# Performance work log

Measured on AMD Instinct MI355X. Metric: run time of the kernel, lower is better.

Reference implementation:

```python
import jax, jax.numpy as jnp
import numpy as np


def _gather_neighbours(h, idx):
    # h: (B, N, H); idx: (B, N, K) int -> (B, N, K, H)
    B, N, H = h.shape
    K = idx.shape[-1]
    flat = idx.reshape(B, N * K)  # (B, N*K)
    rep = jnp.take_along_axis(h, flat[..., None], axis=1)  # (B, N*K, H)
    return rep.reshape(B, N, K, H)


def _masked_agg(h, idx, mask):
    # gather neighbor hidden states then masked sum over neighbors -> (B, N, H)
    rep = _gather_neighbours(h, idx)
    return jnp.einsum('bnkh,bnk->bnh', rep, mask)


def setup_inputs() -> dict:
    key = jax.random.key(0)
    ks = jax.random.split(key, 12)
    B, N, H, K = 8, 2000, 128, 32
    s = 1.0 / np.sqrt(H)
    return {
        'node_hidden': jax.random.normal(ks[0], (B, N, H), jnp.float32),
        'cell': jax.random.normal(ks[1], (B, N, H), jnp.float32),
        'w_in': jax.random.normal(ks[2], (4, H, H), jnp.float32) * s,
        'w_out': jax.random.normal(ks[3], (4, H, H), jnp.float32) * s,
        'u_in': jax.random.normal(ks[4], (4, H, H), jnp.float32) * s,
        'u_out': jax.random.normal(ks[5], (4, H, H), jnp.float32) * s,
        'b': jax.random.normal(ks[6], (4, H), jnp.float32) * 0.1,
        'in_node_mask': jax.random.uniform(ks[7], (B, N, K), jnp.float32),
        'out_node_mask': jax.random.uniform(ks[8], (B, N, K), jnp.float32),
        'in_node_index': jax.random.randint(ks[9], (B, N, K), 0, N, jnp.int32),
        'out_node_index': jax.random.randint(ks[10], (B, N, K), 0, N, jnp.int32),
        'layer_num': 2,
    }


def reference(node_hidden, cell, w_in, w_out, u_in, u_out, b,
              in_node_mask, out_node_mask, in_node_index, out_node_index,
              layer_num):
    h, c = node_hidden, cell
    for _ in range(layer_num):
        in_agg = _masked_agg(h, in_node_index, in_node_mask)    # (B,N,H)
        out_agg = _masked_agg(h, out_node_index, out_node_mask)  # (B,N,H)
        # gate pre-activations, gate order: i, o, f, cell
        pre = (jnp.einsum('bnh,ghd->gbnd', in_agg, w_in)
               + jnp.einsum('bnh,ghd->gbnd', out_agg, w_out)
               + jnp.einsum('bnh,ghd->gbnd', h, u_in)
               + jnp.einsum('bnh,ghd->gbnd', h, u_out)
               + b[:, None, None, :])
        i_g = jax.nn.sigmoid(pre[0])
        o_g = jax.nn.sigmoid(pre[1])
        f_g = jax.nn.sigmoid(pre[2])
        g = jnp.tanh(pre[3])
        c = f_g * c + i_g * g
        h = o_g * jnp.tanh(c)
    return h
```

## Files before the change

kernel.cpp:

```cpp
#include <hip/hip_runtime.h>
#include <math.h>

#define B_ 8
#define N_ 2000
#define H_ 128
#define K_ 32
#define M_ (B_*N_)
#define KTOT 384
#define NC 512
#define NTILES 32
#define NCHUNK 12
#define AGG_BLOCKS (M_ / 8)
#define PREP_BLOCKS (NTILES * NCHUNK)

typedef __attribute__((ext_vector_type(8))) short s8_t;
typedef __attribute__((ext_vector_type(4))) float f4_t;

__device__ __forceinline__ unsigned short f2bf(float x) {
    union { float f; unsigned u; } v; v.f = x;
    unsigned r = v.u + 0x7fff + ((v.u >> 16) & 1);
    return (unsigned short)(r >> 16);
}
__device__ __forceinline__ float bf2f(unsigned short b) {
    union { unsigned u; float f; } v; v.u = (unsigned)b << 16; return v.f;
}
__device__ __forceinline__ float sigm_(float x) { return 1.f / (1.f + __expf(-x)); }
__device__ __forceinline__ float tanh_(float x) { return 2.f / (1.f + __expf(-2.f * x)) - 1.f; }

__device__ __forceinline__ float pickv(f4_t A, int m) {
    float ab = (m & 1) ? A.y : A.x;
    float cd = (m & 1) ? A.w : A.z;
    return (m & 2) ? cd : ab;
}
__device__ __forceinline__ float pick4(float u0, float u1, float u2, float u3, int m) {
    float ab = (m & 1) ? u1 : u0;
    float cd = (m & 1) ? u3 : u2;
    return (m & 2) ? cd : ab;
}

__device__ __forceinline__ void split4(const float* f, ushort4& hi, ushort4& lo) {
    unsigned short h0 = f2bf(f[0]), h1 = f2bf(f[1]), h2 = f2bf(f[2]), h3 = f2bf(f[3]);
    hi = make_ushort4(h0, h1, h2, h3);
    lo = make_ushort4(f2bf(f[0] - bf2f(h0)), f2bf(f[1] - bf2f(h1)),
                      f2bf(f[2] - bf2f(h2)), f2bf(f[3] - bf2f(h3)));
}

__device__ __forceinline__ void gload_lds(const unsigned short* g, short* l) {
    __builtin_amdgcn_global_load_lds(
        (const __attribute__((address_space(1))) unsigned*)g,
        (__attribute__((address_space(3))) unsigned*)l, 16, 0, 0);
}


__device__ __forceinline__ void prep_elem(int pb, int t,
                                          const float* __restrict__ w_in,
                                          const float* __restrict__ w_out,
                                          const float* __restrict__ u_in,
                                          const float* __restrict__ u_out,
                                          unsigned short* __restrict__ wp_hi,
                                          unsigned short* __restrict__ wp_lo) {
    int ntile = pb / NCHUNK, chunk = pb % NCHUNK;
    int lane = t >> 3, e = t & 7;
    int col = ntile * 16 + (lane & 15);
    int k = chunk * 32 + (lane >> 4) * 8 + e;
    int d = col >> 2, g = col & 3;
    float v;
    if (k < 128) {
        v = w_in[(g * 128 + k) * 128 + d];
    } else if (k < 256) {
        v = w_out[(g * 128 + (k - 128)) * 128 + d];
    } else {
        int kk = k - 256;
        v = u_in[(g * 128 + kk) * 128 + d] + u_out[(g * 128 + kk) * 128 + d];
    }
    unsigned short hs = f2bf(v);
    wp_hi[(size_t)pb * 512 + t] = hs;
    wp_lo[(size_t)pb * 512 + t] = f2bf(v - bf2f(hs));
}

__device__ __forceinline__ void agg_body(int bid, int tid,
                                         const float* __restrict__ h,
                                         const int* __restrict__ in_idx,
                                         const float* __restrict__ in_mask,
                                         const int* __restrict__ out_idx,
                                         const float* __restrict__ out_mask,
                                         unsigned short* __restrict__ A_hi,
                                         unsigned short* __restrict__ A_lo,
                                         int (*s_idx)[64], float (*s_msk)[64]) {
    int r = tid >> 5;
    int p = tid & 31;
    int row = bid * 8 + r;
    int b = row / N_;
    const float* hb = h + (size_t)b * N_ * H_;

    for (int e = tid; e < 512; e += 256) {
        int r2 = e >> 6, q = e & 63;
        int ridx = bid * 8 + r2;
        if (q < 32) {
            s_idx[r2][q] = in_idx[ridx * K_ + q];
            s_msk[r2][q] = in_mask[ridx * K_ + q];
        } else {
            s_idx[r2][q] = out_idx[ridx * K_ + (q - 32)];
            s_msk[r2][q] = out_mask[ridx * K_ + (q - 32)];
        }
    }
    __syncthreads();

    int d0 = p * 4;
    float ai[4] = {0.f, 0.f, 0.f, 0.f};
    float ao[4] = {0.f, 0.f, 0.f, 0.f};
    #pragma unroll 16
    for (int k = 0; k < K_; ++k) {
        int   i1 = s_idx[r][k];
        float m1 = s_msk[r][k];
        int   i2 = s_idx[r][32 + k];
        float m2 = s_msk[r][32 + k];
        float4 v1 = *(const float4*)(hb + (size_t)i1 * H_ + d0);
        float4 v2 = *(const float4*)(hb + (size_t)i2 * H_ + d0);
        ai[0] += m1 * v1.x; ai[1] += m1 * v1.y; ai[2] += m1 * v1.z; ai[3] += m1 * v1.w;
        ao[0] += m2 * v2.x; ao[1] += m2 * v2.y; ao[2] += m2 * v2.z; ao[3] += m2 * v2.w;
    }
    float4 hv4 = *(const float4*)(h + (size_t)row * H_ + d0);
    float hh[4] = {hv4.x, hv4.y, hv4.z, hv4.w};

    int mtile = row >> 4;
    int kg = (p >> 1) & 3;
    int e0 = (p & 1) * 4;
    int lane = (row & 15) + 16 * kg;
    size_t bi = ((size_t)(mtile * NCHUNK +     (p >> 3)) * 64 + lane) * 8 + e0;
    size_t bo = ((size_t)(mtile * NCHUNK + 4 + (p >> 3)) * 64 + lane) * 8 + e0;
    size_t bh = ((size_t)(mtile * NCHUNK + 8 + (p >> 3)) * 64 + lane) * 8 + e0;

    ushort4 hi, lo;
    split4(ai, hi, lo); *(ushort4*)(A_hi + bi) = hi; *(ushort4*)(A_lo + bi) = lo;
    split4(ao, hi, lo); *(ushort4*)(A_hi + bo) = hi; *(ushort4*)(A_lo + bo) = lo;
    split4(hh, hi, lo); *(ushort4*)(A_hi + bh) = hi; *(ushort4*)(A_lo + bh) = lo;
}

__global__ __launch_bounds__(256)
void agg0_prep_kernel(const float* __restrict__ h,
                      const int* __restrict__ in_idx,
                      const float* __restrict__ in_mask,
                      const int* __restrict__ out_idx,
                      const float* __restrict__ out_mask,
                      unsigned short* __restrict__ A_hi,
                      unsigned short* __restrict__ A_lo,
                      const float* __restrict__ w_in,
                      const float* __restrict__ w_out,
                      const float* __restrict__ u_in,
                      const float* __restrict__ u_out,
                      unsigned short* __restrict__ wp_hi,
                      unsigned short* __restrict__ wp_lo) {
    __shared__ int   s_idx[8][64];
    __shared__ float s_msk[8][64];
    int tid = threadIdx.x;
    if (blockIdx.x < AGG_BLOCKS) {
        int bid = (blockIdx.x & 7) * 250 + (blockIdx.x >> 3);
        agg_body(bid, tid, h, in_idx, in_mask, out_idx, out_mask,
                 A_hi, A_lo, s_idx, s_msk);
    } else {
        int pb = blockIdx.x - AGG_BLOCKS;
        prep_elem(pb, tid,       w_in, w_out, u_in, u_out, wp_hi, wp_lo);
        prep_elem(pb, tid + 256, w_in, w_out, u_in, u_out, wp_hi, wp_lo);
    }
}

__global__ __launch_bounds__(256)
void agg_kernel(const float* __restrict__ h,
                const int* __restrict__ in_idx,
                const float* __restrict__ in_mask,
                const int* __restrict__ out_idx,
                const float* __restrict__ out_mask,
                unsigned short* __restrict__ A_hi,
                unsigned short* __restrict__ A_lo) {
    __shared__ int   s_idx[8][64];
    __shared__ float s_msk[8][64];
    int bid = (blockIdx.x & 7) * 250 + (blockIdx.x >> 3);
    agg_body(bid, threadIdx.x, h, in_idx, in_mask, out_idx, out_mask,
             A_hi, A_lo, s_idx, s_msk);
}

__global__ __launch_bounds__(256)
void gemm_gates(const unsigned short* __restrict__ A_hi,
                const unsigned short* __restrict__ A_lo,
                const unsigned short* __restrict__ wp_hi,
                const unsigned short* __restrict__ wp_lo,
                const float* __restrict__ bias,
                const float* __restrict__ c_src,
                float* __restrict__ c_dst,
                float* __restrict__ h_dst,
                int write_c) {
    __shared__ short sL[32 * 512];
    int tid  = threadIdx.x;
    int mt   = blockIdx.x;
    int jt   = blockIdx.y;
    int lane = tid & 63;
    int w    = tid >> 6;
    int wm   = w & 1;
    int wn   = w >> 1;
    int mtile0 = mt * 8;
    int ntile0 = jt * 8;

    const unsigned short* gp[8];
    short* lp[8];
    #pragma unroll
    for (int i = 0; i < 8; ++i) {
        int s = i * 4 + w;
        const unsigned short* src;
        if (s < 8)       src = A_hi  + ((size_t)((mtile0 + s)      * NCHUNK) * 64 + lane) * 8;
        else if (s < 16) src = A_lo  + ((size_t)((mtile0 + s - 8)  * NCHUNK) * 64 + lane) * 8;
        else if (s < 24) src = wp_hi + ((size_t)((ntile0 + s - 16) * NCHUNK) * 64 + lane) * 8;
        else             src = wp_lo + ((size_t)((ntile0 + s - 24) * NCHUNK) * 64 + lane) * 8;
        gp[i] = src;
        lp[i] = &sL[s * 512];
    }

    f4_t zero = {0.f, 0.f, 0.f, 0.f};
    f4_t acc[4][4];
    #pragma unroll
    for (int i = 0; i < 4; ++i)
        #pragma unroll
        for (int j = 0; j < 4; ++j) acc[i][j] = zero;

    #pragma unroll 1
    for (int c = 0; c < NCHUNK; ++c) {
        if (c > 0) __syncthreads();
        #pragma unroll
        for (int i = 0; i < 8; ++i) {
            gload_lds(gp[i], lp[i]);
            gp[i] += 512;
        }
        __syncthreads();

        s8_t a_hi[4], a_lo[4], b_hi[4], b_lo[4];
        #pragma unroll
        for (int i = 0; i < 4; ++i) {
            a_hi[i] = *(const s8_t*)&sL[(wm * 4 + i) * 512 + lane * 8];
            a_lo[i] = *(const s8_t*)&sL[(8 + wm * 4 + i) * 512 + lane * 8];
        }
        #pragma unroll
        for (int j = 0; j < 4; ++j) {
            b_hi[j] = *(const s8_t*)&sL[(16 + wn * 4 + j) * 512 + lane * 8];
            b_lo[j] = *(const s8_t*)&sL[(24 + wn * 4 + j) * 512 + lane * 8];
        }
        #pragma unroll
        for (int i = 0; i < 4; ++i)
            #pragma unroll
            for (int j = 0; j < 4; ++j) {
                acc[i][j] = __builtin_amdgcn_mfma_f32_16x16x32_bf16(a_hi[i], b_hi[j], acc[i][j], 0, 0, 0);
                acc[i][j] = __builtin_amdgcn_mfma_f32_16x16x32_bf16(a_hi[i], b_lo[j], acc[i][j], 0, 0, 0);
                acc[i][j] = __builtin_amdgcn_mfma_f32_16x16x32_bf16(a_lo[i], b_hi[j], acc[i][j], 0, 0, 0);
            }
    }

    int g    = lane & 3;
    int qrow = lane >> 4;
    int dl   = (lane >> 2) & 3;
    #pragma unroll
    for (int j = 0; j < 4; ++j) {
        int ncol_base = jt * 128 + wn * 64 + j * 16;
        int d = (ncol_base >> 2) + dl;
        float b0 = bias[0 * 128 + d];
        float b1 = bias[1 * 128 + d];
        float b2 = bias[2 * 128 + d];
        float b3 = bias[3 * 128 + d];
        #pragma unroll
        for (int i = 0; i < 4; ++i) {
            f4_t A = acc[i][j];
            float s0 = pickv(A, g);
            float s1 = pickv(A, g ^ 1);
            float s2 = pickv(A, g ^ 2);
            float s3 = pickv(A, g ^ 3);
            float u0 = s0;
            float u1 = __shfl_xor(s1, 1);
            float u2 = __shfl_xor(s2, 2);
            float u3 = __shfl_xor(s3, 3);
            float p0 = pick4(u0, u1, u2, u3, g) + b0;
            float p1 = pick4(u0, u1, u2, u3, g ^ 1) + b1;
            float p2 = pick4(u0, u1, u2, u3, g ^ 2) + b2;
            float p3 = pick4(u0, u1, u2, u3, g ^ 3) + b3;
            float ig = sigm_(p0);
            float og = sigm_(p1);
            float fg = sigm_(p2);
            float cg = tanh_(p3);
            int row = mt * 128 + wm * 64 + i * 16 + qrow * 4 + g;
            size_t off = (size_t)row * H_ + d;
            float c_old = c_src[off];
            float c_new = fg * c_old + ig * cg;
            if (write_c) c_dst[off] = c_new;
            h_dst[off] = og * tanh_(c_new);
        }
    }
}

extern "C" void kernel_launch(void* const* d_in, const int* in_sizes, int n_in,
                              void* d_out, int out_size, void* d_ws, size_t ws_size,
                              hipStream_t stream) {
    const float* node_hidden = (const float*)d_in[0];
    const float* cell        = (const float*)d_in[1];
    const float* w_in        = (const float*)d_in[2];
    const float* w_out       = (const float*)d_in[3];
    const float* u_in        = (const float*)d_in[4];
    const float* u_out       = (const float*)d_in[5];
    const float* bias        = (const float*)d_in[6];
    const float* in_mask     = (const float*)d_in[7];
    const float* out_mask    = (const float*)d_in[8];
    const int*   in_idx      = (const int*)d_in[9];
    const int*   out_idx     = (const int*)d_in[10];
    float* out = (float*)d_out;

    char* p = (char*)d_ws;
    unsigned short* wp_hi = (unsigned short*)p; p += (size_t)NTILES * NCHUNK * 512 * 2;
    unsigned short* wp_lo = (unsigned short*)p; p += (size_t)NTILES * NCHUNK * 512 * 2;
    unsigned short* A_hi  = (unsigned short*)p; p += (size_t)(M_/16) * NCHUNK * 512 * 2;
    unsigned short* A_lo  = (unsigned short*)p; p += (size_t)(M_/16) * NCHUNK * 512 * 2;
    float* h_buf = (float*)p;                   p += (size_t)M_ * H_ * 4;

    agg0_prep_kernel<<<AGG_BLOCKS + PREP_BLOCKS, 256, 0, stream>>>(
        node_hidden, in_idx, in_mask, out_idx, out_mask, A_hi, A_lo,
        w_in, w_out, u_in, u_out, wp_hi, wp_lo);
    gemm_gates<<<dim3(M_ / 128, 4), 256, 0, stream>>>(
        A_hi, A_lo, wp_hi, wp_lo, bias, cell, out, h_buf, 1);

    agg_kernel<<<AGG_BLOCKS, 256, 0, stream>>>(h_buf, in_idx, in_mask,
                                               out_idx, out_mask, A_hi, A_lo);
    gemm_gates<<<dim3(M_ / 128, 4), 256, 0, stream>>>(
        A_hi, A_lo, wp_hi, wp_lo, bias, out, out, out, 0);
}
```

Before: 192.9 us.

## Fuse all four stages into one cooperative persistent kernel with grid syncs

Replaces the four kernel launches (agg+prep, gemm, agg, gemm) with a single cooperative kernel of 512 blocks that loops over aggregation rows and GEMM tiles, using grid.sync between stages. The aim is to remove launch gaps and tail effects between the dependent stages. In exchange, each stage runs with a fixed grid, so the GEMM covers its 500 tiles with only 512 blocks and aggregation is serialized per block. Grid barriers add their own cost. If the cooperative launch fails, it falls back to the original multi-kernel path.

```diff
diff --git a/kernel.cpp b/kernel.cpp
--- a/kernel.cpp
+++ b/kernel.cpp
@@ -1,5 +1,8 @@
 #include <hip/hip_runtime.h>
+#include <hip/hip_cooperative_groups.h>
 #include <math.h>
+
+namespace cg = cooperative_groups;
 
 #define B_ 8
 #define N_ 2000
@@ -12,6 +15,7 @@
 #define NCHUNK 12
 #define AGG_BLOCKS (M_ / 8)
 #define PREP_BLOCKS (NTILES * NCHUNK)
+#define GRID_ 512
 
 typedef __attribute__((ext_vector_type(8))) short s8_t;
 typedef __attribute__((ext_vector_type(4))) float f4_t;
@@ -50,7 +54,6 @@
         (const __attribute__((address_space(1))) unsigned*)g,
         (__attribute__((address_space(3))) unsigned*)l, 16, 0, 0);
 }
-
 
 __device__ __forceinline__ void prep_elem(int pb, int t,
                                           const float* __restrict__ w_in,
@@ -78,7 +81,7 @@
     wp_lo[(size_t)pb * 512 + t] = f2bf(v - bf2f(hs));
 }
 
-__device__ __forceinline__ void agg_body(int bid, int tid,
+__device__ __forceinline__ void agg_body(int a, int tid,
                                          const float* __restrict__ h,
                                          const int* __restrict__ in_idx,
                                          const float* __restrict__ in_mask,
@@ -89,13 +92,13 @@
                                          int (*s_idx)[64], float (*s_msk)[64]) {
     int r = tid >> 5;
     int p = tid & 31;
-    int row = bid * 8 + r;
+    int row = a * 8 + r;
     int b = row / N_;
     const float* hb = h + (size_t)b * N_ * H_;
 
     for (int e = tid; e < 512; e += 256) {
         int r2 = e >> 6, q = e & 63;
-        int ridx = bid * 8 + r2;
+        int ridx = a * 8 + r2;
         if (q < 32) {
             s_idx[r2][q] = in_idx[ridx * K_ + q];
             s_msk[r2][q] = in_mask[ridx * K_ + q];
@@ -135,6 +138,177 @@
     split4(ai, hi, lo); *(ushort4*)(A_hi + bi) = hi; *(ushort4*)(A_lo + bi) = lo;
     split4(ao, hi, lo); *(ushort4*)(A_hi + bo) = hi; *(ushort4*)(A_lo + bo) = lo;
     split4(hh, hi, lo); *(ushort4*)(A_hi + bh) = hi; *(ushort4*)(A_lo + bh) = lo;
+}
+
+__device__ __forceinline__ void gemm_body(int mt, int jt, int tid, short* sL,
+                const unsigned short* __restrict__ A_hi,
+                const unsigned short* __restrict__ A_lo,
+                const unsigned short* __restrict__ wp_hi,
+                const unsigned short* __restrict__ wp_lo,
+                const float* __restrict__ bias,
+                const float* __restrict__ c_src,
+                float* __restrict__ c_dst,
+                float* __restrict__ h_dst,
+                int write_c) {
+    int lane = tid & 63;
+    int w    = tid >> 6;
+    int wm   = w & 1;
+    int wn   = w >> 1;
+    int mtile0 = mt * 8;
+    int ntile0 = jt * 8;
+
+    const unsigned short* gp[8];
+    short* lp[8];
+    #pragma unroll
+    for (int i = 0; i < 8; ++i) {
+        int s = i * 4 + w;
+        const unsigned short* src;
+        if (s < 8)       src = A_hi  + ((size_t)((mtile0 + s)      * NCHUNK) * 64 + lane) * 8;
+        else if (s < 16) src = A_lo  + ((size_t)((mtile0 + s - 8)  * NCHUNK) * 64 + lane) * 8;
+        else if (s < 24) src = wp_hi + ((size_t)((ntile0 + s - 16) * NCHUNK) * 64 + lane) * 8;
+        else             src = wp_lo + ((size_t)((ntile0 + s - 24) * NCHUNK) * 64 + lane) * 8;
+        gp[i] = src;
+        lp[i] = &sL[s * 512];
+    }
+
+    f4_t zero = {0.f, 0.f, 0.f, 0.f};
+    f4_t acc[4][4];
+    #pragma unroll
+    for (int i = 0; i < 4; ++i)
+        #pragma unroll
+        for (int j = 0; j < 4; ++j) acc[i][j] = zero;
+
+    #pragma unroll 1
+    for (int c = 0; c < NCHUNK; ++c) {
+        __syncthreads();
+        #pragma unroll
+        for (int i = 0; i < 8; ++i) {
+            gload_lds(gp[i], lp[i]);
+            gp[i] += 512;
+        }
+        __syncthreads();
+
+        s8_t a_hi[4], a_lo[4], b_hi[4], b_lo[4];
+        #pragma unroll
+        for (int i = 0; i < 4; ++i) {
+            a_hi[i] = *(const s8_t*)&sL[(wm * 4 + i) * 512 + lane * 8];
+            a_lo[i] = *(const s8_t*)&sL[(8 + wm * 4 + i) * 512 + lane * 8];
+        }
+        #pragma unroll
+        for (int j = 0; j < 4; ++j) {
+            b_hi[j] = *(const s8_t*)&sL[(16 + wn * 4 + j) * 512 + lane * 8];
+            b_lo[j] = *(const s8_t*)&sL[(24 + wn * 4 + j) * 512 + lane * 8];
+        }
+        #pragma unroll
+        for (int i = 0; i < 4; ++i)
+            #pragma unroll
+            for (int j = 0; j < 4; ++j) {
+                acc[i][j] = __builtin_amdgcn_mfma_f32_16x16x32_bf16(a_hi[i], b_hi[j], acc[i][j], 0, 0, 0);
+                acc[i][j] = __builtin_amdgcn_mfma_f32_16x16x32_bf16(a_hi[i], b_lo[j], acc[i][j], 0, 0, 0);
+                acc[i][j] = __builtin_amdgcn_mfma_f32_16x16x32_bf16(a_lo[i], b_hi[j], acc[i][j], 0, 0, 0);
+            }
+    }
+
+    int g    = lane & 3;
+    int qrow = lane >> 4;
+    int dl   = (lane >> 2) & 3;
+    #pragma unroll
+    for (int j = 0; j < 4; ++j) {
+        int ncol_base = jt * 128 + wn * 64 + j * 16;
+        int d = (ncol_base >> 2) + dl;
+        float b0 = bias[0 * 128 + d];
+        float b1 = bias[1 * 128 + d];
+        float b2 = bias[2 * 128 + d];
+        float b3 = bias[3 * 128 + d];
+        #pragma unroll
+        for (int i = 0; i < 4; ++i) {
+            f4_t A = acc[i][j];
+            float s0 = pickv(A, g);
+            float s1 = pickv(A, g ^ 1);
+            float s2 = pickv(A, g ^ 2);
+            float s3 = pickv(A, g ^ 3);
+            float u0 = s0;
+            float u1 = __shfl_xor(s1, 1);
+            float u2 = __shfl_xor(s2, 2);
+            float u3 = __shfl_xor(s3, 3);
+            float p0 = pick4(u0, u1, u2, u3, g) + b0;
+            float p1 = pick4(u0, u1, u2, u3, g ^ 1) + b1;
+            float p2 = pick4(u0, u1, u2, u3, g ^ 2) + b2;
+            float p3 = pick4(u0, u1, u2, u3, g ^ 3) + b3;
+            float ig = sigm_(p0);
+            float og = sigm_(p1);
+            float fg = sigm_(p2);
+            float cg = tanh_(p3);
+            int row = mt * 128 + wm * 64 + i * 16 + qrow * 4 + g;
+            size_t off = (size_t)row * H_ + d;
+            float c_old = c_src[off];
+            float c_new = fg * c_old + ig * cg;
+            if (write_c) c_dst[off] = c_new;
+            h_dst[off] = og * tanh_(c_new);
+        }
+    }
+}
+
+__global__ __launch_bounds__(256, 2)
+void fused_all(const float* __restrict__ node_hidden,
+               const float* __restrict__ cell,
+               const float* __restrict__ w_in,
+               const float* __restrict__ w_out,
+               const float* __restrict__ u_in,
+               const float* __restrict__ u_out,
+               const float* __restrict__ bias,
+               const float* __restrict__ in_mask,
+               const float* __restrict__ out_mask,
+               const int* __restrict__ in_idx,
+               const int* __restrict__ out_idx,
+               unsigned short* __restrict__ wp_hi,
+               unsigned short* __restrict__ wp_lo,
+               unsigned short* __restrict__ A_hi,
+               unsigned short* __restrict__ A_lo,
+               float* __restrict__ h_buf,
+               float* __restrict__ out) {
+    __shared__ short sL[32 * 512];
+    cg::grid_group grid = cg::this_grid();
+    int tid = threadIdx.x;
+    int pb  = blockIdx.x;
+    int x   = pb & 7;
+    int sl  = pb >> 3;
+
+    int (*s_idx)[64] = (int(*)[64])sL;
+    float (*s_msk)[64] = (float(*)[64])(sL + 1024);
+
+    int glo = (125 * x + 7) >> 3;
+    int ghi = (125 * (x + 1) + 7) >> 3;
+    int gcnt = (ghi - glo) * 4;
+    int gmt = glo + (sl >> 2);
+    int gjt = sl & 3;
+
+    if (pb < PREP_BLOCKS) {
+        prep_elem(pb, tid,       w_in, w_out, u_in, u_out, wp_hi, wp_lo);
+        prep_elem(pb, tid + 256, w_in, w_out, u_in, u_out, wp_hi, wp_lo);
+    }
+    for (int q = sl; q < 250; q += 64) {
+        agg_body(x * 250 + q, tid, node_hidden, in_idx, in_mask,
+                 out_idx, out_mask, A_hi, A_lo, s_idx, s_msk);
+        __syncthreads();
+    }
+    grid.sync();
+
+    if (sl < gcnt)
+        gemm_body(gmt, gjt, tid, sL, A_hi, A_lo, wp_hi, wp_lo, bias,
+                  cell, out, h_buf, 1);
+    grid.sync();
+
+    for (int q = sl; q < 250; q += 64) {
+        agg_body(x * 250 + q, tid, h_buf, in_idx, in_mask,
+                 out_idx, out_mask, A_hi, A_lo, s_idx, s_msk);
+        __syncthreads();
+    }
+    grid.sync();
+
+    if (sl < gcnt)
+        gemm_body(gmt, gjt, tid, sL, A_hi, A_lo, wp_hi, wp_lo, bias,
+                  out, out, out, 0);
 }
 
 __global__ __launch_bounds__(256)
@@ -191,106 +365,8 @@
                 float* __restrict__ h_dst,
                 int write_c) {
     __shared__ short sL[32 * 512];
-    int tid  = threadIdx.x;
-    int mt   = blockIdx.x;
-    int jt   = blockIdx.y;
-    int lane = tid & 63;
-    int w    = tid >> 6;
-    int wm   = w & 1;
-    int wn   = w >> 1;
-    int mtile0 = mt * 8;
-    int ntile0 = jt * 8;
-
-    const unsigned short* gp[8];
-    short* lp[8];
-    #pragma unroll
-    for (int i = 0; i < 8; ++i) {
-        int s = i * 4 + w;
-        const unsigned short* src;
-        if (s < 8)       src = A_hi  + ((size_t)((mtile0 + s)      * NCHUNK) * 64 + lane) * 8;
-        else if (s < 16) src = A_lo  + ((size_t)((mtile0 + s - 8)  * NCHUNK) * 64 + lane) * 8;
-        else if (s < 24) src = wp_hi + ((size_t)((ntile0 + s - 16) * NCHUNK) * 64 + lane) * 8;
-        else             src = wp_lo + ((size_t)((ntile0 + s - 24) * NCHUNK) * 64 + lane) * 8;
-        gp[i] = src;
-        lp[i] = &sL[s * 512];
-    }
-
-    f4_t zero = {0.f, 0.f, 0.f, 0.f};
-    f4_t acc[4][4];
-    #pragma unroll
-    for (int i = 0; i < 4; ++i)
-        #pragma unroll
-        for (int j = 0; j < 4; ++j) acc[i][j] = zero;
-
-    #pragma unroll 1
-    for (int c = 0; c < NCHUNK; ++c) {
-        if (c > 0) __syncthreads();
-        #pragma unroll
-        for (int i = 0; i < 8; ++i) {
-            gload_lds(gp[i], lp[i]);
-            gp[i] += 512;
-        }
-        __syncthreads();
-
-        s8_t a_hi[4], a_lo[4], b_hi[4], b_lo[4];
-        #pragma unroll
-        for (int i = 0; i < 4; ++i) {
-            a_hi[i] = *(const s8_t*)&sL[(wm * 4 + i) * 512 + lane * 8];
-            a_lo[i] = *(const s8_t*)&sL[(8 + wm * 4 + i) * 512 + lane * 8];
-        }
-        #pragma unroll
-        for (int j = 0; j < 4; ++j) {
-            b_hi[j] = *(const s8_t*)&sL[(16 + wn * 4 + j) * 512 + lane * 8];
-            b_lo[j] = *(const s8_t*)&sL[(24 + wn * 4 + j) * 512 + lane * 8];
-        }
-        #pragma unroll
-        for (int i = 0; i < 4; ++i)
-            #pragma unroll
-            for (int j = 0; j < 4; ++j) {
-                acc[i][j] = __builtin_amdgcn_mfma_f32_16x16x32_bf16(a_hi[i], b_hi[j], acc[i][j], 0, 0, 0);
-                acc[i][j] = __builtin_amdgcn_mfma_f32_16x16x32_bf16(a_hi[i], b_lo[j], acc[i][j], 0, 0, 0);
-                acc[i][j] = __builtin_amdgcn_mfma_f32_16x16x32_bf16(a_lo[i], b_hi[j], acc[i][j], 0, 0, 0);
-            }
-    }
-
-    int g    = lane & 3;
-    int qrow = lane >> 4;
-    int dl   = (lane >> 2) & 3;
-    #pragma unroll
-    for (int j = 0; j < 4; ++j) {
-        int ncol_base = jt * 128 + wn * 64 + j * 16;
-        int d = (ncol_base >> 2) + dl;
-        float b0 = bias[0 * 128 + d];
-        float b1 = bias[1 * 128 + d];
-        float b2 = bias[2 * 128 + d];
-        float b3 = bias[3 * 128 + d];
-        #pragma unroll
-        for (int i = 0; i < 4; ++i) {
-            f4_t A = acc[i][j];
-            float s0 = pickv(A, g);
-            float s1 = pickv(A, g ^ 1);
-            float s2 = pickv(A, g ^ 2);
-            float s3 = pickv(A, g ^ 3);
-            float u0 = s0;
-            float u1 = __shfl_xor(s1, 1);
-            float u2 = __shfl_xor(s2, 2);
-            float u3 = __shfl_xor(s3, 3);
-            float p0 = pick4(u0, u1, u2, u3, g) + b0;
-            float p1 = pick4(u0, u1, u2, u3, g ^ 1) + b1;
-            float p2 = pick4(u0, u1, u2, u3, g ^ 2) + b2;
-            float p3 = pick4(u0, u1, u2, u3, g ^ 3) + b3;
-            float ig = sigm_(p0);
-            float og = sigm_(p1);
-            float fg = sigm_(p2);
-            float cg = tanh_(p3);
-            int row = mt * 128 + wm * 64 + i * 16 + qrow * 4 + g;
-            size_t off = (size_t)row * H_ + d;
-            float c_old = c_src[off];
-            float c_new = fg * c_old + ig * cg;
-            if (write_c) c_dst[off] = c_new;
-            h_dst[off] = og * tanh_(c_new);
-        }
-    }
+    gemm_body(blockIdx.x, blockIdx.y, threadIdx.x, sL,
+              A_hi, A_lo, wp_hi, wp_lo, bias, c_src, c_dst, h_dst, write_c);
 }
 
 extern "C" void kernel_launch(void* const* d_in, const int* in_sizes, int n_in,
@@ -316,14 +392,25 @@
     unsigned short* A_lo  = (unsigned short*)p; p += (size_t)(M_/16) * NCHUNK * 512 * 2;
     float* h_buf = (float*)p;                   p += (size_t)M_ * H_ * 4;
 
-    agg0_prep_kernel<<<AGG_BLOCKS + PREP_BLOCKS, 256, 0, stream>>>(
-        node_hidden, in_idx, in_mask, out_idx, out_mask, A_hi, A_lo,
-        w_in, w_out, u_in, u_out, wp_hi, wp_lo);
-    gemm_gates<<<dim3(M_ / 128, 4), 256, 0, stream>>>(
-        A_hi, A_lo, wp_hi, wp_lo, bias, cell, out, h_buf, 1);
-
-    agg_kernel<<<AGG_BLOCKS, 256, 0, stream>>>(h_buf, in_idx, in_mask,
-                                               out_idx, out_mask, A_hi, A_lo);
-    gemm_gates<<<dim3(M_ / 128, 4), 256, 0, stream>>>(
-        A_hi, A_lo, wp_hi, wp_lo, bias, out, out, out, 0);
-}
+    void* args[] = {
+        (void*)&node_hidden, (void*)&cell, (void*)&w_in, (void*)&w_out,
+        (void*)&u_in, (void*)&u_out, (void*)&bias, (void*)&in_mask,
+        (void*)&out_mask, (void*)&in_idx, (void*)&out_idx,
+        (void*)&wp_hi, (void*)&wp_lo, (void*)&A_hi, (void*)&A_lo,
+        (void*)&h_buf, (void*)&out
+    };
+    hipError_t err = hipLaunchCooperativeKernel((const void*)fused_all,
+                                                dim3(GRID_), dim3(256),
+                                                args, 0, stream);
+    if (err != hipSuccess) {
+        agg0_prep_kernel<<<AGG_BLOCKS + PREP_BLOCKS, 256, 0, stream>>>(
+            node_hidden, in_idx, in_mask, out_idx, out_mask, A_hi, A_lo,
+            w_in, w_out, u_in, u_out, wp_hi, wp_lo);
+        gemm_gates<<<dim3(M_ / 128, 4), 256, 0, stream>>>(
+            A_hi, A_lo, wp_hi, wp_lo, bias, cell, out, h_buf, 1);
+        agg_kernel<<<AGG_BLOCKS, 256, 0, stream>>>(h_buf, in_idx, in_mask,
+                                                   out_idx, out_mask, A_hi, A_lo);
+        gemm_gates<<<dim3(M_ / 128, 4), 256, 0, stream>>>(
+            A_hi, A_lo, wp_hi, wp_lo, bias, out, out, out, 0);
+    }
+}
```

Measured after the change: 435.5 us. 126% more time.
